# Optimization experiments

Measured on AMD Instinct MI355X. Metric: run time of the kernel, lower is better.

The kernel has to match this reference:

```python
import jax, jax.numpy as jnp
import numpy as np

EPS = 1e-08


def setup_inputs() -> dict:
    key = jax.random.key(0)
    k1, k2 = jax.random.split(key)
    N, D, C = 8192, 512, 1000
    features = jax.random.uniform(k1, (N, D), dtype=jnp.float32)
    logits = jax.random.normal(k2, (N, C), dtype=jnp.float32)
    return {"features": features, "logits": logits}


def reference(features, logits):
    N = features.shape[0]
    # softmax over classes, plus eps (matches F.softmax(...) + eps)
    p = jax.nn.softmax(logits, axis=1) + EPS                     # [N, C]
    # similarity matrix with diagonal removed
    cos_sim = features @ features.T - jnp.eye(N, dtype=features.dtype)  # [N, N]
    neighbor_mask = (cos_sim >= -1).astype(cos_sim.dtype)
    w = cos_sim * neighbor_mask
    w = w / jnp.sum(w, axis=1, keepdims=True)                    # row-normalized weights
    weighted_sum_nb = w @ p                                      # [N, C]
    # F.kl_div(log_input, target, reduction='batchmean')
    # = sum(target * (log(target) - log_input)) / N
    kl = jnp.sum(weighted_sum_nb * (jnp.log(weighted_sum_nb) - jnp.log(p))) / N
    return kl
```

## Files before the change

### kernel.cpp

```cpp
#include <hip/hip_runtime.h>
#include <math.h>

#define NN 8192
#define DD 512
#define CC 1000
#define CP 1024
#define CPD (CP*DD)

typedef __attribute__((ext_vector_type(8))) short short8;
typedef __attribute__((ext_vector_type(4))) float f32x4;
typedef __attribute__((ext_vector_type(4))) unsigned short us4;
typedef __attribute__((ext_vector_type(8))) unsigned short us8;

__device__ __forceinline__ float bf2f(unsigned short u){
  union{unsigned int i; float f;} v; v.i = ((unsigned int)u)<<16; return v.f;
}
__device__ __forceinline__ unsigned short f2bf(float f){
  union{float f; unsigned int i;} v; v.f = f;
  unsigned int r = v.i + 0x7FFF + ((v.i>>16)&1);
  return (unsigned short)(r>>16);
}
__device__ __forceinline__ float waveRedSum(float v){
  #pragma unroll
  for(int o=32;o;o>>=1) v += __shfl_xor(v,o,64);
  return v;
}
__device__ __forceinline__ float waveRedMax(float v){
  #pragma unroll
  for(int o=32;o;o>>=1) v = fmaxf(v,__shfl_xor(v,o,64));
  return v;
}
__device__ __forceinline__ void gload_lds16(const void* g, void* l){
  __builtin_amdgcn_global_load_lds((const __attribute__((address_space(1))) void*)g,
                                   (__attribute__((address_space(3))) void*)l, 16, 0, 0);
}

__global__ __launch_bounds__(256) void k_prep(const float* __restrict__ F,
                                              const float* __restrict__ L,
                                              unsigned short* __restrict__ FbT,
                                              unsigned short* __restrict__ Fb,
                                              float* __restrict__ gpart,
                                              unsigned short* __restrict__ PbT,
                                              float* __restrict__ out){
  __shared__ __align__(16) char smem[16*1032*2];
  int bid = blockIdx.x;
  int grp = bid/3, r = bid - grp*3;
  int t = threadIdx.x;
  if(bid==0 && t==0) out[0] = 0.f;

  if(r < 2){
    int cb = grp*2 + r;
    unsigned short* lds = (unsigned short*)smem;
    float* gq = (float*)(smem + 64*68*2);
    int i0 = (cb & 127)*64, d0 = (cb >> 7)*64;
    int cx = t&15, ry = t>>4;
    float ca0=0.f,ca1=0.f,ca2=0.f,ca3=0.f;
    #pragma unroll
    for(int rr=0;rr<4;rr++){
      int row = rr*16 + ry;
      f32x4 fv = *(const f32x4*)&F[(size_t)(i0+row)*DD + d0 + cx*4];
      us4 u; u[0]=f2bf(fv[0]); u[1]=f2bf(fv[1]); u[2]=f2bf(fv[2]); u[3]=f2bf(fv[3]);
      *(us4*)&lds[row*68 + cx*4] = u;
      *(us4*)&Fb[(size_t)(i0+row)*DD + d0 + cx*4] = u;
      ca0+=fv[0]; ca1+=fv[1]; ca2+=fv[2]; ca3+=fv[3];
    }
    {
      f32x4 cv; cv[0]=ca0; cv[1]=ca1; cv[2]=ca2; cv[3]=ca3;
      *(f32x4*)&gq[ry*64 + cx*4] = cv;
    }
    __syncthreads();
    #pragma unroll
    for(int rr=0;rr<4;rr++){
      int d = rr*16 + ry;
      us4 u;
      #pragma unroll
      for(int q=0;q<4;q++) u[q] = lds[(cx*4+q)*68 + d];
      *(us4*)&FbT[(size_t)(d0+d)*NN + i0 + cx*4] = u;
    }
    __syncthreads();
    if(t<64){
      float s=0.f;
      #pragma unroll
      for(int j=0;j<16;j++) s += gq[j*64+t];
      gpart[(cb&127)*DD + d0 + t] = s;
    }
  } else {
    int sb = grp;
    unsigned short (*lt)[1032] = (unsigned short(*)[1032])smem;
    int l = t&63, w = t>>6;
    int i0 = sb*16;
    #pragma unroll
    for(int q=0;q<4;q++){
      int rr = w*4 + q;
      int row = i0 + rr;
      const float* lr = L + (size_t)row*CC;
      float v[16]; float mx = -1e30f;
      #pragma unroll
      for(int k=0;k<4;k++){
        int c4 = l*4 + 256*k;
        f32x4 fv;
        if(c4 < CC) fv = *(const f32x4*)&lr[c4];
        else { fv[0]=-1e30f; fv[1]=-1e30f; fv[2]=-1e30f; fv[3]=-1e30f; }
        v[4*k+0]=fv[0]; v[4*k+1]=fv[1]; v[4*k+2]=fv[2]; v[4*k+3]=fv[3];
        mx = fmaxf(mx, fmaxf(fmaxf(fv[0],fv[1]), fmaxf(fv[2],fv[3])));
      }
      mx = waveRedMax(mx);
      float s = 0.f;
      #pragma unroll
      for(int e=0;e<16;e++){ v[e] = __expf(v[e]-mx); s += v[e]; }
      s = waveRedSum(s);
      float inv = 1.0f/s;
      #pragma unroll
      for(int k=0;k<4;k++){
        int c4 = l*4 + 256*k;
        us4 u;
        #pragma unroll
        for(int j=0;j<4;j++){
          float p = v[4*k+j]*inv + 1e-8f;
          u[j] = (c4+j < CC)? f2bf(p) : (unsigned short)0;
        }
        *(us4*)&lt[rr][c4] = u;
      }
    }
    __syncthreads();
    #pragma unroll
    for(int k=0;k<4;k++){
      int c = t + 256*k;
      us8 a, b;
      #pragma unroll
      for(int j=0;j<8;j++){ a[j] = lt[j][c]; b[j] = lt[j+8][c]; }
      *(us8*)&PbT[(size_t)c*NN + i0]     = a;
      *(us8*)&PbT[(size_t)c*NN + i0 + 8] = b;
    }
  }
}

__global__ __launch_bounds__(256,2) void k_gemm1(const unsigned short* __restrict__ A,
                                                 const unsigned short* __restrict__ B,
                                                 unsigned short* __restrict__ Tpb,
                                                 const float* __restrict__ gpart,
                                                 float* __restrict__ g){
  __shared__ __align__(16) unsigned short smem[4*8192];
  __shared__ float rs[4][64];
  int bid = blockIdx.x;
  int t = threadIdx.x;
  if(bid < 8){
    int d = bid*64 + (t&63);
    int q = t>>6;
    float s = 0.f;
    #pragma unroll
    for(int j=0;j<32;j++) s += gpart[(size_t)(q*32+j)*DD + d];
    rs[q][t&63] = s;
    __syncthreads();
    if(q==0) g[d] = rs[0][t&63]+rs[1][t&63]+rs[2][t&63]+rs[3][t&63];
    return;
  }
  int gb = bid - 8;
  int Lsw = (gb&7)*64 + (gb>>3);
  int l = t&63, w = t>>6;
  int bx = Lsw & 7, by = (Lsw>>3) & 3, bz = Lsw>>5;
  int m0 = bx*128, n0 = by*128;
  int k0 = bz*512;
  int wm = w>>1, wn = w&1;
  f32x4 acc[4][4] = {};
  int srow = w*32 + (l>>3);
  int scl  = (l&7) ^ (srow&7);
  const unsigned short* Ab = A + (size_t)(m0 + srow)*NN + k0 + scl*8;
  const unsigned short* Bb = B + (size_t)(n0 + srow)*NN + k0 + scl*8;
  int ldsOff = (w*32)*64;

  #pragma unroll
  for(int q=0;q<4;q++){
    gload_lds16(Ab + (size_t)q*8*NN, smem + ldsOff + q*8*64);
    gload_lds16(Bb + (size_t)q*8*NN, smem + 8192 + ldsOff + q*8*64);
  }
  int cur = 0;
  for(int kt=0; kt<512; kt+=64){
    if(kt+64 < 512){
      unsigned short* An = smem + (cur^1)*16384 + ldsOff;
      unsigned short* Bn = smem + (cur^1)*16384 + 8192 + ldsOff;
      #pragma unroll
      for(int q=0;q<4;q++){
        gload_lds16(Ab + (size_t)q*8*NN + kt + 64, An + q*8*64);
        gload_lds16(Bb + (size_t)q*8*NN + kt + 64, Bn + q*8*64);
      }
      asm volatile("s_waitcnt vmcnt(8)" ::: "memory");
    } else {
      asm volatile("s_waitcnt vmcnt(0)" ::: "memory");
    }
    __builtin_amdgcn_s_barrier();
    const unsigned short* Ac = smem + cur*16384;
    const unsigned short* Bc = smem + cur*16384 + 8192;
    #pragma unroll
    for(int ks=0;ks<2;ks++){
      short8 af[4], bf[4];
      #pragma unroll
      for(int mi=0;mi<4;mi++){
        int rr = wm*64 + mi*16 + (l&15);
        int ch = ((ks<<2) + (l>>4)) ^ (rr&7);
        af[mi] = *(const short8*)&Ac[rr*64 + ch*8];
      }
      #pragma unroll
      for(int ni=0;ni<4;ni++){
        int rr = wn*64 + ni*16 + (l&15);
        int ch = ((ks<<2) + (l>>4)) ^ (rr&7);
        bf[ni] = *(const short8*)&Bc[rr*64 + ch*8];
      }
      #pragma unroll
      for(int mi=0;mi<4;mi++)
        #pragma unroll
        for(int ni=0;ni<4;ni++)
          acc[mi][ni] = __builtin_amdgcn_mfma_f32_16x16x32_bf16(af[mi], bf[ni], acc[mi][ni], 0,0,0);
    }
    __builtin_amdgcn_s_barrier();
    cur ^= 1;
  }
  unsigned short* Tz = Tpb + (size_t)bz*CPD;
  int rbase = (l>>4)*4;
  #pragma unroll
  for(int mi=0;mi<4;mi++){
    int c = m0 + wm*64 + mi*16 + rbase;
    #pragma unroll
    for(int ni=0;ni<4;ni++){
      int d = n0 + wn*64 + ni*16 + (l&15);
      #pragma unroll
      for(int j=0;j<4;j++)
        Tz[(size_t)(c+j)*DD + d] = f2bf(acc[mi][ni][j]);
    }
  }
}

__global__ __launch_bounds__(256) void k_redT(const unsigned short* __restrict__ Tpb,
                                              const unsigned short* __restrict__ Fb,
                                              const float* __restrict__ g,
                                              unsigned short* __restrict__ Ttb,
                                              float* __restrict__ invr){
  int t = threadIdx.x;
  size_t i = ((size_t)blockIdx.x*256 + (size_t)t)*8;
  f32x4 s0 = {0.f,0.f,0.f,0.f}, s1 = {0.f,0.f,0.f,0.f};
  #pragma unroll
  for(int z=0;z<16;z++){
    us8 v = *(const us8*)&Tpb[(size_t)z*CPD + i];
    s0[0]+=bf2f(v[0]); s0[1]+=bf2f(v[1]); s0[2]+=bf2f(v[2]); s0[3]+=bf2f(v[3]);
    s1[0]+=bf2f(v[4]); s1[1]+=bf2f(v[5]); s1[2]+=bf2f(v[6]); s1[3]+=bf2f(v[7]);
  }
  us8 u;
  u[0]=f2bf(s0[0]); u[1]=f2bf(s0[1]); u[2]=f2bf(s0[2]); u[3]=f2bf(s0[3]);
  u[4]=f2bf(s1[0]); u[5]=f2bf(s1[1]); u[6]=f2bf(s1[2]); u[7]=f2bf(s1[3]);
  *(us8*)&Ttb[i] = u;
  int row = blockIdx.x*32 + (t>>3);
  int seg = (t&7)*64;
  const unsigned short* fr = Fb + (size_t)row*DD + seg;
  const float* gr = g + seg;
  float s = 0.f;
  #pragma unroll
  for(int j=0;j<8;j++){
    us8 f8 = *(const us8*)&fr[j*8];
    f32x4 ga = *(const f32x4*)&gr[j*8];
    f32x4 gb = *(const f32x4*)&gr[j*8+4];
    s += bf2f(f8[0])*ga[0]+bf2f(f8[1])*ga[1]+bf2f(f8[2])*ga[2]+bf2f(f8[3])*ga[3]
       + bf2f(f8[4])*gb[0]+bf2f(f8[5])*gb[1]+bf2f(f8[6])*gb[2]+bf2f(f8[7])*gb[3];
  }
  s += __shfl_xor(s,1,64); s += __shfl_xor(s,2,64); s += __shfl_xor(s,4,64);
  if((t&7)==0) invr[row] = 1.0f/(s - 1.0f);
}

__global__ __launch_bounds__(256,2) void k_gemm2(const unsigned short* __restrict__ Fb,
                                                 const unsigned short* __restrict__ Bt,
                                                 const unsigned short* __restrict__ PbT,
                                                 const float* __restrict__ invr,
                                                 float* __restrict__ out){
  __shared__ __align__(16) unsigned short smem[4*8192];
  __shared__ float red[4];
  int bid = blockIdx.x;
  int Lsw = (bid&7)*64 + (bid>>3);
  int t = threadIdx.x, l = t&63, w = t>>6;
  int m0 = (Lsw>>3)*128, n0 = (Lsw&7)*128;
  int wm = w>>1, wn = w&1;
  f32x4 acc[4][4] = {};
  int srow = w*32 + (l>>3);
  int scl  = (l&7) ^ (srow&7);
  const unsigned short* Ab = Fb + (size_t)(m0 + srow)*DD + scl*8;
  const unsigned short* Bb = Bt + (size_t)(n0 + srow)*DD + scl*8;
  int ldsOff = (w*32)*64;

  #pragma unroll
  for(int q=0;q<4;q++){
    gload_lds16(Ab + (size_t)q*8*DD, smem + ldsOff + q*8*64);
    gload_lds16(Bb + (size_t)q*8*DD, smem + 8192 + ldsOff + q*8*64);
  }
  int cur = 0;
  for(int kt=0; kt<512; kt+=64){
    if(kt+64 < 512){
      unsigned short* An = smem + (cur^1)*16384 + ldsOff;
      unsigned short* Bn = smem + (cur^1)*16384 + 8192 + ldsOff;
      #pragma unroll
      for(int q=0;q<4;q++){
        gload_lds16(Ab + (size_t)q*8*DD + kt + 64, An + q*8*64);
        gload_lds16(Bb + (size_t)q*8*DD + kt + 64, Bn + q*8*64);
      }
      asm volatile("s_waitcnt vmcnt(8)" ::: "memory");
    } else {
      asm volatile("s_waitcnt vmcnt(0)" ::: "memory");
    }
    __builtin_amdgcn_s_barrier();
    const unsigned short* Ac = smem + cur*16384;
    const unsigned short* Bc = smem + cur*16384 + 8192;
    #pragma unroll
    for(int ks=0;ks<2;ks++){
      short8 af[4], bf[4];
      #pragma unroll
      for(int mi=0;mi<4;mi++){
        int rr = wm*64 + mi*16 + (l&15);
        int ch = ((ks<<2) + (l>>4)) ^ (rr&7);
        af[mi] = *(const short8*)&Ac[rr*64 + ch*8];
      }
      #pragma unroll
      for(int ni=0;ni<4;ni++){
        int rr = wn*64 + ni*16 + (l&15);
        int ch = ((ks<<2) + (l>>4)) ^ (rr&7);
        bf[ni] = *(const short8*)&Bc[rr*64 + ch*8];
      }
      #pragma unroll
      for(int mi=0;mi<4;mi++)
        #pragma unroll
        for(int ni=0;ni<4;ni++)
          acc[mi][ni] = __builtin_amdgcn_mfma_f32_16x16x32_bf16(af[mi], bf[ni], acc[mi][ni], 0,0,0);
    }
    __builtin_amdgcn_s_barrier();
    cur ^= 1;
  }
  __syncthreads();
  #pragma unroll
  for(int j=0;j<8;j++){
    int e = j*256 + t;
    int row = e >> 4;
    int ch  = e & 15;
    us8 v = *(const us8*)&PbT[(size_t)(n0+row)*NN + m0 + ch*8];
    *(us8*)&smem[row*136 + ch*8] = v;
  }
  __syncthreads();
  float kl = 0.f;
  int rbase = (l>>4)*4;
  #pragma unroll
  for(int mi=0;mi<4;mi++){
    int i_base = m0 + wm*64 + mi*16 + rbase;
    int ci = wm*64 + mi*16 + rbase;
    f32x4 ir4 = *(const f32x4*)&invr[i_base];
    #pragma unroll
    for(int ni=0;ni<4;ni++){
      int cr = wn*64 + ni*16 + (l&15);
      int c = n0 + cr;
      if(c < CC){
        us4 p4 = *(const us4*)&smem[cr*136 + ci];
        #pragma unroll
        for(int j=0;j<4;j++){
          float p = bf2f(p4[j]);
          float ws = (acc[mi][ni][j] - p) * ir4[j];
          kl += ws * (__logf(ws) - __logf(p));
        }
      }
    }
  }
  kl = waveRedSum(kl);
  if(l==0) red[w]=kl;
  __syncthreads();
  if(t==0) atomicAdd(out, (red[0]+red[1]+red[2]+red[3]) * (1.0f/(float)NN));
}

extern "C" void kernel_launch(void* const* d_in, const int* in_sizes, int n_in,
                              void* d_out, int out_size, void* d_ws, size_t ws_size,
                              hipStream_t stream){
  const float* F = (const float*)d_in[0];
  const float* L = (const float*)d_in[1];
  float* out = (float*)d_out;

  unsigned char* w8 = (unsigned char*)d_ws;
  unsigned short* FbT = (unsigned short*)w8;
  unsigned short* PbT = (unsigned short*)(w8 + (8u<<20));
  unsigned short* Tpb = (unsigned short*)(w8 + (24u<<20));
  unsigned short* Ttb = (unsigned short*)(w8 + (40u<<20));
  unsigned short* Fb  = (unsigned short*)(w8 + (41u<<20));
  float* gpart        = (float*)(w8 + (49u<<20));
  float* g            = (float*)(w8 + (49u<<20) + 262144);
  float* invr         = (float*)(w8 + (49u<<20) + 264192);

  hipLaunchKernelGGL(k_prep,  dim3(1536), dim3(256), 0, stream, F, L, FbT, Fb, gpart, PbT, out);
  hipLaunchKernelGGL(k_gemm1, dim3(520),  dim3(256), 0, stream, PbT, FbT, Tpb, gpart, g);
  hipLaunchKernelGGL(k_redT,  dim3(256),  dim3(256), 0, stream, Tpb, Fb, g, Ttb, invr);
  hipLaunchKernelGGL(k_gemm2, dim3(512),  dim3(256), 0, stream, Fb, Ttb, PbT, invr, out);
}
```

Baseline: 66.94 us.

## Fuse split-K reduction into gemm1 via last-block counter, compute row norms in gemm2

Removes the separate k_redT kernel. The split-K partial reduction now runs inside gemm1: for each output tile, the last of the 16 z-blocks to finish (tracked by an atomic counter that k_prep resets) sums the bf16 partials and writes Ttb. The inverse row sums are now computed per tile at the start of gemm2 from Fb and g and kept in LDS. This saves one launch and its sync gap, at the cost of redundant row-sum work in each gemm2 block and a serialized reduction tail on the last-arriving blocks.

```diff
diff --git a/kernel.cpp b/kernel.cpp
--- a/kernel.cpp
+++ b/kernel.cpp
@@ -41,12 +41,16 @@
                                               unsigned short* __restrict__ Fb,
                                               float* __restrict__ gpart,
                                               unsigned short* __restrict__ PbT,
+                                              int* __restrict__ cnt,
                                               float* __restrict__ out){
   __shared__ __align__(16) char smem[16*1032*2];
   int bid = blockIdx.x;
   int grp = bid/3, r = bid - grp*3;
   int t = threadIdx.x;
-  if(bid==0 && t==0) out[0] = 0.f;
+  if(bid==0){
+    if(t<32) cnt[t] = 0;
+    if(t==32) out[0] = 0.f;
+  }
 
   if(r < 2){
     int cb = grp*2 + r;
@@ -87,7 +91,8 @@
   } else {
     int sb = grp;
     unsigned short (*lt)[1032] = (unsigned short(*)[1032])smem;
-    int l = t&63, w = t>>6;
+    int l = t&63;
+    int w = t>>6;
     int i0 = sb*16;
     #pragma unroll
     for(int q=0;q<4;q++){
@@ -139,9 +144,12 @@
                                                  const unsigned short* __restrict__ B,
                                                  unsigned short* __restrict__ Tpb,
                                                  const float* __restrict__ gpart,
-                                                 float* __restrict__ g){
+                                                 float* __restrict__ g,
+                                                 unsigned short* __restrict__ Ttb,
+                                                 int* __restrict__ cnt){
   __shared__ __align__(16) unsigned short smem[4*8192];
   __shared__ float rs[4][64];
+  __shared__ int redflag;
   int bid = blockIdx.x;
   int t = threadIdx.x;
   if(bid < 8){
@@ -228,50 +236,44 @@
         Tz[(size_t)(c+j)*DD + d] = f2bf(acc[mi][ni][j]);
     }
   }
-}
-
-__global__ __launch_bounds__(256) void k_redT(const unsigned short* __restrict__ Tpb,
-                                              const unsigned short* __restrict__ Fb,
-                                              const float* __restrict__ g,
-                                              unsigned short* __restrict__ Ttb,
-                                              float* __restrict__ invr){
-  int t = threadIdx.x;
-  size_t i = ((size_t)blockIdx.x*256 + (size_t)t)*8;
-  f32x4 s0 = {0.f,0.f,0.f,0.f}, s1 = {0.f,0.f,0.f,0.f};
-  #pragma unroll
-  for(int z=0;z<16;z++){
-    us8 v = *(const us8*)&Tpb[(size_t)z*CPD + i];
-    s0[0]+=bf2f(v[0]); s0[1]+=bf2f(v[1]); s0[2]+=bf2f(v[2]); s0[3]+=bf2f(v[3]);
-    s1[0]+=bf2f(v[4]); s1[1]+=bf2f(v[5]); s1[2]+=bf2f(v[6]); s1[3]+=bf2f(v[7]);
-  }
-  us8 u;
-  u[0]=f2bf(s0[0]); u[1]=f2bf(s0[1]); u[2]=f2bf(s0[2]); u[3]=f2bf(s0[3]);
-  u[4]=f2bf(s1[0]); u[5]=f2bf(s1[1]); u[6]=f2bf(s1[2]); u[7]=f2bf(s1[3]);
-  *(us8*)&Ttb[i] = u;
-  int row = blockIdx.x*32 + (t>>3);
-  int seg = (t&7)*64;
-  const unsigned short* fr = Fb + (size_t)row*DD + seg;
-  const float* gr = g + seg;
-  float s = 0.f;
-  #pragma unroll
-  for(int j=0;j<8;j++){
-    us8 f8 = *(const us8*)&fr[j*8];
-    f32x4 ga = *(const f32x4*)&gr[j*8];
-    f32x4 gb = *(const f32x4*)&gr[j*8+4];
-    s += bf2f(f8[0])*ga[0]+bf2f(f8[1])*ga[1]+bf2f(f8[2])*ga[2]+bf2f(f8[3])*ga[3]
-       + bf2f(f8[4])*gb[0]+bf2f(f8[5])*gb[1]+bf2f(f8[6])*gb[2]+bf2f(f8[7])*gb[3];
-  }
-  s += __shfl_xor(s,1,64); s += __shfl_xor(s,2,64); s += __shfl_xor(s,4,64);
-  if((t&7)==0) invr[row] = 1.0f/(s - 1.0f);
+  __syncthreads();
+  if(t==0){
+    __threadfence();
+    int old = atomicAdd(&cnt[by*8+bx], 1);
+    redflag = (old==15);
+  }
+  __syncthreads();
+  if(!redflag) return;
+  __threadfence();
+  #pragma unroll
+  for(int rr=0;rr<4;rr++){
+    int row = rr*32 + (t>>3);
+    int dc  = (t&7)*16;
+    size_t base = (size_t)(m0+row)*DD + n0 + dc;
+    float a0[8] = {0,0,0,0,0,0,0,0}, a1[8] = {0,0,0,0,0,0,0,0};
+    #pragma unroll
+    for(int z=0;z<16;z++){
+      us8 v0 = *(const us8*)&Tpb[(size_t)z*CPD + base];
+      us8 v1 = *(const us8*)&Tpb[(size_t)z*CPD + base + 8];
+      #pragma unroll
+      for(int j=0;j<8;j++){ a0[j] += bf2f(v0[j]); a1[j] += bf2f(v1[j]); }
+    }
+    us8 o0, o1;
+    #pragma unroll
+    for(int j=0;j<8;j++){ o0[j] = f2bf(a0[j]); o1[j] = f2bf(a1[j]); }
+    *(us8*)&Ttb[base]     = o0;
+    *(us8*)&Ttb[base + 8] = o1;
+  }
 }
 
 __global__ __launch_bounds__(256,2) void k_gemm2(const unsigned short* __restrict__ Fb,
                                                  const unsigned short* __restrict__ Bt,
                                                  const unsigned short* __restrict__ PbT,
-                                                 const float* __restrict__ invr,
+                                                 const float* __restrict__ g,
                                                  float* __restrict__ out){
   __shared__ __align__(16) unsigned short smem[4*8192];
   __shared__ float red[4];
+  __shared__ float invrL[128];
   int bid = blockIdx.x;
   int Lsw = (bid&7)*64 + (bid>>3);
   int t = threadIdx.x, l = t&63, w = t>>6;
@@ -289,6 +291,27 @@
     gload_lds16(Ab + (size_t)q*8*DD, smem + ldsOff + q*8*64);
     gload_lds16(Bb + (size_t)q*8*DD, smem + 8192 + ldsOff + q*8*64);
   }
+  {
+    int rlocal = t>>4;
+    int dseg = (t&15)*32;
+    #pragma unroll
+    for(int rr=0;rr<8;rr++){
+      int row = rr*16 + rlocal;
+      const unsigned short* fr = Fb + (size_t)(m0+row)*DD + dseg;
+      float s = 0.f;
+      #pragma unroll
+      for(int j=0;j<4;j++){
+        us8 f8 = *(const us8*)&fr[j*8];
+        f32x4 ga = *(const f32x4*)&g[dseg + j*8];
+        f32x4 gb = *(const f32x4*)&g[dseg + j*8 + 4];
+        s += bf2f(f8[0])*ga[0]+bf2f(f8[1])*ga[1]+bf2f(f8[2])*ga[2]+bf2f(f8[3])*ga[3]
+           + bf2f(f8[4])*gb[0]+bf2f(f8[5])*gb[1]+bf2f(f8[6])*gb[2]+bf2f(f8[7])*gb[3];
+      }
+      s += __shfl_xor(s,1,64); s += __shfl_xor(s,2,64);
+      s += __shfl_xor(s,4,64); s += __shfl_xor(s,8,64);
+      if((t&15)==0) invrL[row] = 1.0f/(s - 1.0f);
+    }
+  }
   int cur = 0;
   for(int kt=0; kt<512; kt+=64){
     if(kt+64 < 512){
@@ -344,9 +367,8 @@
   int rbase = (l>>4)*4;
   #pragma unroll
   for(int mi=0;mi<4;mi++){
-    int i_base = m0 + wm*64 + mi*16 + rbase;
     int ci = wm*64 + mi*16 + rbase;
-    f32x4 ir4 = *(const f32x4*)&invr[i_base];
+    f32x4 ir4 = *(const f32x4*)&invrL[ci];
     #pragma unroll
     for(int ni=0;ni<4;ni++){
       int cr = wn*64 + ni*16 + (l&15);
@@ -383,10 +405,9 @@
   unsigned short* Fb  = (unsigned short*)(w8 + (41u<<20));
   float* gpart        = (float*)(w8 + (49u<<20));
   float* g            = (float*)(w8 + (49u<<20) + 262144);
-  float* invr         = (float*)(w8 + (49u<<20) + 264192);
-
-  hipLaunchKernelGGL(k_prep,  dim3(1536), dim3(256), 0, stream, F, L, FbT, Fb, gpart, PbT, out);
-  hipLaunchKernelGGL(k_gemm1, dim3(520),  dim3(256), 0, stream, PbT, FbT, Tpb, gpart, g);
-  hipLaunchKernelGGL(k_redT,  dim3(256),  dim3(256), 0, stream, Tpb, Fb, g, Ttb, invr);
-  hipLaunchKernelGGL(k_gemm2, dim3(512),  dim3(256), 0, stream, Fb, Ttb, PbT, invr, out);
-}
+  int*   cnt          = (int*)  (w8 + (49u<<20) + 264192);
+
+  hipLaunchKernelGGL(k_prep,  dim3(1536), dim3(256), 0, stream, F, L, FbT, Fb, gpart, PbT, cnt, out);
+  hipLaunchKernelGGL(k_gemm1, dim3(520),  dim3(256), 0, stream, PbT, FbT, Tpb, gpart, g, Ttb, cnt);
+  hipLaunchKernelGGL(k_gemm2, dim3(512),  dim3(256), 0, stream, Fb, Ttb, PbT, g, out);
+}
```

Result: slower. 115.6 us (+72.8%).
